# Kernel optimization log

Measured on AMD Instinct MI355X. Metric: run time of the kernel, lower is better.

The kernel has to match this reference:

```python
import jax, jax.numpy as jnp
import numpy as np

B, N, D = 16, 1024, 1152
H = 16; DH = D // H
GH = GW = 32; SY = SX = 2
WS = SY * SX                      # tokens per window
NW = (GH // SY) * (GW // SX)      # 256 windows (one dst each)
NS = NW * (WS - 1)                # 768 src tokens
NUM_PRUNE = int(N * 0.5)          # 512
NOISE_ALPHA = 0.1
SIM_BETA = 1.0


def setup_inputs() -> dict:
    key = jax.random.key(0)
    ks = jax.random.split(key, 8)
    rn = lambda k, s: jax.random.normal(k, s, jnp.float32) * 0.02
    return dict(
        x=jax.random.normal(ks[0], (B, N, D), jnp.float32),
        noise=jax.random.uniform(ks[1], (B, NW, WS), jnp.float32),
        ln1_g=jnp.ones((D,), jnp.float32), ln1_b=jnp.zeros((D,), jnp.float32),
        ln2_g=jnp.ones((D,), jnp.float32), ln2_b=jnp.zeros((D,), jnp.float32),
        w_qkv=rn(ks[2], (D, 3 * D)), b_qkv=jnp.zeros((3 * D,), jnp.float32),
        w_proj=rn(ks[3], (D, D)), b_proj=jnp.zeros((D,), jnp.float32),
        w_fc1=rn(ks[4], (D, 4 * D)), b_fc1=jnp.zeros((4 * D,), jnp.float32),
        w_fc2=rn(ks[5], (4 * D, D)), b_fc2=jnp.zeros((D,), jnp.float32),
    )


def _ln(x, g, b):
    mu = x.mean(-1, keepdims=True)
    var = ((x - mu) ** 2).mean(-1, keepdims=True)
    return (x - mu) * jax.lax.rsqrt(var + 1e-6) * g + b


def _dit_block(x, ln1_g, ln1_b, ln2_g, ln2_b, w_qkv, b_qkv, w_proj, b_proj,
               w_fc1, b_fc1, w_fc2, b_fc2):
    Bq, T, _ = x.shape
    y = _ln(x, ln1_g, ln1_b)
    q, k, v = jnp.split(y @ w_qkv + b_qkv, 3, axis=-1)
    hd = lambda t: t.reshape(Bq, T, H, DH).transpose(0, 2, 1, 3)  # [B,H,T,DH]
    q, k, v = hd(q), hd(k), hd(v)
    att = jax.nn.softmax(jnp.einsum('bhqd,bhkd->bhqk', q, k) * (1.0 / np.sqrt(DH)), axis=-1)
    o = jnp.einsum('bhqk,bhkd->bhqd', att, v).transpose(0, 2, 1, 3).reshape(Bq, T, D)
    x = x + o @ w_proj + b_proj
    y = _ln(x, ln2_g, ln2_b)
    return x + jax.nn.gelu(y @ w_fc1 + b_fc1) @ w_fc2 + b_fc2


def _sito_indices(x, noise):
    # SiTo seed (dst) selection + similarity-based prune index computation.
    xn = x / (jnp.linalg.norm(x, axis=-1, keepdims=True) + 1e-6)  # cosine feats
    grid = jnp.arange(N).reshape(GH, GW)
    win = grid.reshape(GH // SY, SY, GW // SX, SX).transpose(0, 2, 1, 3).reshape(NW, WS)
    xw = xn[:, win]                                   # [B,NW,WS,D]
    mean = xw.mean(2, keepdims=True)
    score = SIM_BETA * (xw * mean).sum(-1) + NOISE_ALPHA * noise  # [B,NW,WS]
    dst_local = jnp.argmax(score, axis=-1)            # [B,NW]
    winb = jnp.broadcast_to(win, (B, NW, WS))
    dst_idx = jnp.take_along_axis(winb, dst_local[..., None], -1)[..., 0]  # [B,NW]
    local = jnp.arange(WS)[None, None]
    keymat = jnp.where(local != dst_local[..., None], local, WS)
    src_local = jnp.sort(keymat, -1)[..., : WS - 1]   # non-dst locals, in order
    src_idx = jnp.take_along_axis(winb, src_local, -1).reshape(B, NS)
    a = jnp.take_along_axis(xn, src_idx[..., None], 1)      # [B,NS,D]
    bf = jnp.take_along_axis(xn, dst_idx[..., None], 1)     # [B,NW,D]
    sim = jnp.einsum('bsd,bnd->bsn', a, bf)                 # [B,NS,NW]
    best = jnp.argmax(sim, -1)                              # most-similar dst
    order = jnp.argsort(-jnp.max(sim, -1), axis=-1)
    pruned_pos = order[:, :NUM_PRUNE]
    kept_pos = order[:, NUM_PRUNE:]
    src_kept = jnp.take_along_axis(src_idx, kept_pos, 1)
    src_pruned = jnp.take_along_axis(src_idx, pruned_pos, 1)
    pruned_best = jnp.take_along_axis(best, pruned_pos, 1)
    return dst_idx, src_kept, src_pruned, pruned_best


def reference(x, noise, ln1_g, ln1_b, ln2_g, ln2_b, w_qkv, b_qkv, w_proj, b_proj,
              w_fc1, b_fc1, w_fc2, b_fc2):
    dst_idx, src_kept, src_pruned, pruned_best = _sito_indices(x, noise)
    keep_idx = jnp.concatenate([dst_idx, src_kept], axis=1)          # [B,Nk]
    xk = jnp.take_along_axis(x, keep_idx[..., None], 1)              # prune_fn
    out = _dit_block(xk, ln1_g, ln1_b, ln2_g, ln2_b, w_qkv, b_qkv,
                     w_proj, b_proj, w_fc1, b_fc1, w_fc2, b_fc2)

    def recover_one(o, di, sk, sp, pb):  # recover_fn: scatter + copy-from-dst
        out_dst, out_src = o[:NW], o[NW:]
        full = jnp.zeros((N, D), o.dtype)
        full = full.at[di].set(out_dst)
        full = full.at[sk].set(out_src)
        return full.at[sp].set(out_dst[pb])

    return jax.vmap(recover_one)(out, dst_idx, src_kept, src_pruned, pruned_best)
```

## Files before the change

### kernel.cpp

```cpp
#include <hip/hip_runtime.h>
#include <hip/hip_bf16.h>

namespace {

constexpr int Dd = 1152;

typedef __attribute__((ext_vector_type(8))) short bf16x8;
typedef __attribute__((ext_vector_type(4))) float f32x4;

__device__ __forceinline__ void gload_lds16(const void* g, void* l) {
  __builtin_amdgcn_global_load_lds(
      (const __attribute__((address_space(1))) void*)g,
      (__attribute__((address_space(3))) void*)l, 16, 0, 0);
}

__device__ __forceinline__ float gelu_f(float x) {
  float x3 = x * x * x;
  float z2 = 1.5957691216057308f * (x + 0.044715f * x3);
  float e = __expf(fminf(z2, 30.0f));
  return x * e / (e + 1.0f);
}

__global__ __launch_bounds__(256) void normwin_kernel(const float* __restrict__ x,
    const float* __restrict__ noise, float* __restrict__ inv,
    __hip_bfloat16* __restrict__ xnh, __hip_bfloat16* __restrict__ xnl,
    int* __restrict__ dsti, int* __restrict__ srci) {
  const int gidx = blockIdx.x;
  const int b = gidx >> 8, w = gidx & 255;
  const int wy = w >> 4, wx = w & 15;
  const int t0 = wy * 64 + wx * 2;
  const int wid = threadIdx.x >> 6, lane = threadIdx.x & 63;
  const int tok = t0 + (wid >> 1) * 32 + (wid & 1);
  const int row = (b << 10) + tok;

  const float2* xr = (const float2*)(x + (size_t)row * Dd);
  float2 v[9];
  float s = 0.f;
  #pragma unroll
  for (int e = 0; e < 9; ++e) {
    v[e] = xr[lane + 64 * e];
    s += v[e].x * v[e].x + v[e].y * v[e].y;
  }
  #pragma unroll
  for (int m = 1; m < 64; m <<= 1) s += __shfl_xor(s, m);
  float iv = 1.0f / (sqrtf(s) + 1e-6f);
  if (lane == 0) inv[row] = iv;

  __shared__ float2 xns[4][576];
  ushort2* ph = (ushort2*)(xnh + (size_t)row * Dd);
  ushort2* pl = (ushort2*)(xnl + (size_t)row * Dd);
  #pragma unroll
  for (int e = 0; e < 9; ++e) {
    float ax = v[e].x * iv, ay = v[e].y * iv;
    xns[wid][lane + 64 * e] = make_float2(ax, ay);
    __hip_bfloat16 hx = __float2bfloat16(ax), hy = __float2bfloat16(ay);
    __hip_bfloat16 lx = __float2bfloat16(ax - __bfloat162float(hx));
    __hip_bfloat16 ly = __float2bfloat16(ay - __bfloat162float(hy));
    ph[lane + 64 * e] = make_ushort2(*(ushort*)&hx, *(ushort*)&hy);
    pl[lane + 64 * e] = make_ushort2(*(ushort*)&lx, *(ushort*)&ly);
  }
  __syncthreads();

  float dot = 0.f;
  #pragma unroll
  for (int e = 0; e < 9; ++e) {
    int i = lane + 64 * e;
    float2 a0 = xns[0][i], a1 = xns[1][i], a2 = xns[2][i], a3 = xns[3][i];
    float sx = a0.x + a1.x + a2.x + a3.x;
    float sy = a0.y + a1.y + a2.y + a3.y;
    dot += (v[e].x * iv) * sx + (v[e].y * iv) * sy;
  }
  #pragma unroll
  for (int m = 1; m < 64; m <<= 1) dot += __shfl_xor(dot, m);
  __shared__ float dots[4];
  if (lane == 0) dots[wid] = dot;
  __syncthreads();
  if (threadIdx.x == 0) {
    float best = -1e30f; int bj = 0;
    #pragma unroll
    for (int j = 0; j < 4; ++j) {
      float sc = 0.25f * dots[j] + 0.1f * noise[(size_t)gidx * 4 + j];
      if (sc > best) { best = sc; bj = j; }
    }
    int tk[4] = {t0, t0 + 1, t0 + 32, t0 + 33};
    dsti[b * 256 + w] = tk[bj];
    int m = 0;
    #pragma unroll
    for (int j = 0; j < 4; ++j) if (j != bj) srci[b * 768 + w * 3 + (m++)] = tk[j];
  }
}

__global__ __launch_bounds__(256) void simgemm_kernel(
    const __hip_bfloat16* __restrict__ xnh, const __hip_bfloat16* __restrict__ xnl,
    const int* __restrict__ dsti, const int* __restrict__ srci,
    float* __restrict__ mx, int* __restrict__ best) {
  int b = blockIdx.x / 12;
  int m0 = (blockIdx.x % 12) * 64;
  __shared__ __align__(16) __hip_bfloat16 AsH[2][64 * 32];
  __shared__ __align__(16) __hip_bfloat16 AsL[2][64 * 32];
  __shared__ __align__(16) __hip_bfloat16 BsH[2][256 * 32];
  __shared__ __align__(16) __hip_bfloat16 BsL[2][256 * 32];
  const int tid = threadIdx.x, wid = tid >> 6, lane = tid & 63;
  const int g = lane >> 4, lr = lane & 15;

  const int slotRow = tid >> 2;
  const int colByte = (((tid & 3) ^ ((tid >> 3) & 3)) << 4);
  size_t aRow = (size_t)((b << 10) + srci[b * 768 + m0 + slotRow]) * Dd;
  size_t bRow[4];
  #pragma unroll
  for (int p = 0; p < 4; ++p)
    bRow[p] = (size_t)((b << 10) + dsti[b * 256 + p * 64 + slotRow]) * Dd;
  const char* xh = (const char*)xnh;
  const char* xl = (const char*)xnl;

  auto stage = [&](int buf, int k0) {
    size_t ka = (aRow + k0) * 2 + colByte;
    gload_lds16(xh + ka, (char*)AsH + buf * 4096 + wid * 1024);
    gload_lds16(xl + ka, (char*)AsL + buf * 4096 + wid * 1024);
    #pragma unroll
    for (int p = 0; p < 4; ++p) {
      size_t kb = (bRow[p] + k0) * 2 + colByte;
      gload_lds16(xh + kb, (char*)BsH + buf * 16384 + p * 4096 + wid * 1024);
      gload_lds16(xl + kb, (char*)BsL + buf * 16384 + p * 4096 + wid * 1024);
    }
  };

  f32x4 hh[16], hx[16];
  const f32x4 zf = {0.f, 0.f, 0.f, 0.f};
  #pragma unroll
  for (int nf = 0; nf < 16; ++nf) { hh[nf] = zf; hx[nf] = zf; }

  const int roff = ((g ^ ((lr >> 1) & 3)) << 3);
  stage(0, 0);
  asm volatile("s_waitcnt vmcnt(0)" ::: "memory");
  __syncthreads();
  int buf = 0;
  for (int ks = 0; ks < 36; ++ks) {
    if (ks + 1 < 36) stage(buf ^ 1, (ks + 1) * 32);
    bf16x8 ah = *(const bf16x8*)&AsH[buf][(wid * 16 + lr) * 32 + roff];
    bf16x8 al = *(const bf16x8*)&AsL[buf][(wid * 16 + lr) * 32 + roff];
    #pragma unroll
    for (int nf = 0; nf < 16; ++nf) {
      bf16x8 bh = *(const bf16x8*)&BsH[buf][(nf * 16 + lr) * 32 + roff];
      bf16x8 bl = *(const bf16x8*)&BsL[buf][(nf * 16 + lr) * 32 + roff];
      hh[nf] = __builtin_amdgcn_mfma_f32_16x16x32_bf16(ah, bh, hh[nf], 0, 0, 0);
      hx[nf] = __builtin_amdgcn_mfma_f32_16x16x32_bf16(ah, bl, hx[nf], 0, 0, 0);
      hx[nf] = __builtin_amdgcn_mfma_f32_16x16x32_bf16(al, bh, hx[nf], 0, 0, 0);
    }
    asm volatile("s_waitcnt vmcnt(0)" ::: "memory");
    __syncthreads();
    buf ^= 1;
  }

  #pragma unroll
  for (int j = 0; j < 4; ++j) {
    float bv = -1e30f; int bi = 0;
    #pragma unroll
    for (int nf = 0; nf < 16; ++nf) {
      float v = hh[nf][j] + hx[nf][j];
      if (v > bv) { bv = v; bi = nf * 16 + lr; }
    }
    #pragma unroll
    for (int m = 1; m < 16; m <<= 1) {
      float ov = __shfl_xor(bv, m);
      int oi = __shfl_xor(bi, m);
      if (ov > bv || (ov == bv && oi < bi)) { bv = ov; bi = oi; }
    }
    if (lr == 0) {
      int row = m0 + wid * 16 + g * 4 + j;
      mx[b * 768 + row] = bv;
      best[b * 768 + row] = bi;
    }
  }
}

__global__ __launch_bounds__(256) void rank_kernel(const float* __restrict__ mx,
    const int* __restrict__ best, const int* __restrict__ dsti,
    const int* __restrict__ srci, int* __restrict__ keep, int* __restrict__ srow) {
  int b = blockIdx.x;
  int tid = threadIdx.x;
  __shared__ float smx[768];
  for (int i = tid; i < 768; i += 256) smx[i] = mx[b * 768 + i];
  __syncthreads();
  if (tid < 256) {
    int t = dsti[b * 256 + tid];
    keep[b * 512 + tid] = t;
    srow[b * 1024 + t] = tid;
  }
  for (int i = tid; i < 768; i += 256) {
    float v = smx[i];
    int r = 0;
    for (int s = 0; s < 768; ++s) {
      float u = smx[s];
      r += (u > v) || (u == v && s < i);
    }
    int tok = srci[b * 768 + i];
    if (r >= 512) {
      keep[b * 512 + (r - 256)] = tok;
      srow[b * 1024 + tok] = r - 256;
    } else {
      srow[b * 1024 + tok] = best[b * 768 + i];
    }
  }
}

template<int GATHER>
__global__ __launch_bounds__(256) void ln_kernel(const float* __restrict__ xin,
    const int* __restrict__ keep, const float* __restrict__ gw,
    const float* __restrict__ bw, __hip_bfloat16* __restrict__ yout) {
  int row = blockIdx.x;
  const float* xr;
  if (GATHER) {
    int b = row >> 9, t = row & 511;
    int tok = keep[(b << 9) + t];
    xr = xin + (size_t)((b << 10) + tok) * Dd;
  } else {
    xr = xin + (size_t)row * Dd;
  }
  int tid = threadIdx.x;
  float v[5];
  float s = 0.f, s2 = 0.f;
  #pragma unroll
  for (int e = 0; e < 5; ++e) {
    int i = tid + e * 256;
    float val = (i < Dd) ? xr[i] : 0.f;
    v[e] = val; s += val; s2 += val * val;
  }
  #pragma unroll
  for (int m = 1; m < 64; m <<= 1) { s += __shfl_xor(s, m); s2 += __shfl_xor(s2, m); }
  __shared__ float ps[4], ps2[4];
  int wid = tid >> 6, lane = tid & 63;
  if (lane == 0) { ps[wid] = s; ps2[wid] = s2; }
  __syncthreads();
  s = ps[0] + ps[1] + ps[2] + ps[3];
  s2 = ps2[0] + ps2[1] + ps2[2] + ps2[3];
  constexpr float inv_d = 1.0f / Dd;
  float mu = s * inv_d;
  float var = s2 * inv_d - mu * mu;
  float rstd = rsqrtf(var + 1e-6f);
  __hip_bfloat16* yr = yout + (size_t)row * Dd;
  #pragma unroll
  for (int e = 0; e < 5; ++e) {
    int i = tid + e * 256;
    if (i < Dd) {
      yr[i] = __float2bfloat16((v[e] - mu) * rstd * gw[i] + bw[i]);
    }
  }
}

__global__ __launch_bounds__(256) void wtrans_kernel(const float* __restrict__ w,
    __hip_bfloat16* __restrict__ wT, int K, int N) {
  __shared__ float tile[32][33];
  int nt = N >> 5;
  int tk = blockIdx.x / nt, tn = blockIdx.x % nt;
  int tid = threadIdx.x;
  #pragma unroll
  for (int e = 0; e < 4; ++e) {
    int idx = tid + e * 256;
    int r = idx >> 5, c = idx & 31;
    tile[r][c] = w[(size_t)(tk * 32 + r) * N + tn * 32 + c];
  }
  __syncthreads();
  #pragma unroll
  for (int e = 0; e < 4; ++e) {
    int idx = tid + e * 256;
    int r = idx >> 5, c = idx & 31;
    wT[(size_t)(tn * 32 + r) * K + tk * 32 + c] = __float2bfloat16(tile[c][r]);
  }
}

template<int EPI>
__device__ __forceinline__ void epi_store(void* C, const float* res, int Nd,
                                          size_t row, size_t col, float v) {
  if (EPI == 0) {
    ((__hip_bfloat16*)C)[row * (size_t)Nd + col] = __float2bfloat16(v);
  } else if (EPI == 1) {
    ((float*)C)[row * (size_t)Nd + col] = v + res[row * (size_t)Nd + col];
  } else if (EPI == 2) {
    ((__hip_bfloat16*)C)[row * (size_t)Nd + col] = __float2bfloat16(gelu_f(v));
  }
}

template<int EPI>
__global__ __launch_bounds__(512, 4) void gemm128_kernel(
    const __hip_bfloat16* __restrict__ A, const __hip_bfloat16* __restrict__ BT,
    const float* __restrict__ bias, const float* __restrict__ res,
    void* __restrict__ C, int Md, int Nd, int NdPad, int Kd) {
  constexpr int BM = 128;
  __shared__ __align__(16) __hip_bfloat16 As[3][BM * 32];
  __shared__ __align__(16) __hip_bfloat16 Bs[3][256 * 32];
  const int nb = NdPad >> 8;
  const int q8 = gridDim.x >> 3;
  const int wg = (blockIdx.x & 7) * q8 + (blockIdx.x >> 3);
  const int bm = wg / nb, bnb = wg % nb;
  const int tid = threadIdx.x, wid = tid >> 6, lane = tid & 63;
  const int g = lane >> 4, lr = lane & 15;
  const int wm = wid >> 2, wn = wid & 3;
  const size_t m0 = (size_t)bm * BM, n0 = (size_t)bnb * 256;

  const int trow = tid >> 2;
  const int scol = (((tid & 3) ^ ((tid >> 3) & 3)) << 3);
  const char* Ab = (const char*)A;
  const char* Bb = (const char*)BT;

  auto stage = [&](int slot, int kt) {
    const size_t kb = ((size_t)kt << 5) + scol;
    gload_lds16(Ab + (((m0 + trow) * (size_t)Kd + kb) << 1),
                (char*)As + slot * 8192 + wid * 1024);
    gload_lds16(Bb + (((n0 + trow) * (size_t)Kd + kb) << 1),
                (char*)Bs + slot * 16384 + wid * 1024);
    gload_lds16(Bb + (((n0 + 128 + trow) * (size_t)Kd + kb) << 1),
                (char*)Bs + slot * 16384 + 8192 + wid * 1024);
  };

  f32x4 acc[4][4];
  const f32x4 zf = {0.f, 0.f, 0.f, 0.f};
  #pragma unroll
  for (int mi = 0; mi < 4; ++mi)
    #pragma unroll
    for (int ni = 0; ni < 4; ++ni) acc[mi][ni] = zf;

  const int nk = Kd >> 5;
  stage(0, 0);
  stage(1, 1);
  asm volatile("s_waitcnt vmcnt(3)" ::: "memory");
  __builtin_amdgcn_s_barrier();

  int cur = 0;
  const int roff = ((g ^ ((lr >> 1) & 3)) << 3);
  for (int kt = 0; kt < nk; ++kt) {
    const __hip_bfloat16* Ac = As[cur];
    const __hip_bfloat16* Bc = Bs[cur];
    bf16x8 af[4], bf[4];
    #pragma unroll
    for (int mi = 0; mi < 4; ++mi)
      af[mi] = *(const bf16x8*)&Ac[(wm * 64 + mi * 16 + lr) * 32 + roff];
    #pragma unroll
    for (int ni = 0; ni < 4; ++ni)
      bf[ni] = *(const bf16x8*)&Bc[(wn * 64 + ni * 16 + lr) * 32 + roff];
    if (kt + 2 < nk) stage(cur == 0 ? 2 : cur - 1, kt + 2);
    __builtin_amdgcn_s_barrier();
    __builtin_amdgcn_s_setprio(1);
    #pragma unroll
    for (int mi = 0; mi < 4; ++mi)
      #pragma unroll
      for (int ni = 0; ni < 4; ++ni)
        acc[mi][ni] = __builtin_amdgcn_mfma_f32_16x16x32_bf16(af[mi], bf[ni], acc[mi][ni], 0, 0, 0);
    __builtin_amdgcn_s_setprio(0);
    if (kt + 2 < nk)      asm volatile("s_waitcnt vmcnt(3)" ::: "memory");
    else if (kt + 1 < nk) asm volatile("s_waitcnt vmcnt(0)" ::: "memory");
    __builtin_amdgcn_s_barrier();
    cur = (cur == 2) ? 0 : cur + 1;
  }

  #pragma unroll
  for (int ni = 0; ni < 4; ++ni) {
    size_t col = n0 + wn * 64 + ni * 16 + lr;
    if (col < (size_t)Nd) {
      float bv = bias[col];
      #pragma unroll
      for (int mi = 0; mi < 4; ++mi) {
        #pragma unroll
        for (int j = 0; j < 4; ++j) {
          size_t row = m0 + wm * 64 + mi * 16 + g * 4 + j;
          float v = acc[mi][ni][j] + bv;
          epi_store<EPI>(C, res, Nd, row, col, v);
        }
      }
    }
  }
}

template<int EPI>
__global__ __launch_bounds__(256, 3) void gemm128v_kernel(
    const __hip_bfloat16* __restrict__ A, const __hip_bfloat16* __restrict__ BT,
    const float* __restrict__ bias, const float* __restrict__ res,
    const int* __restrict__ keepIdx, const float* __restrict__ xsrc,
    void* __restrict__ C, int Md, int Nd, int Kd) {
  __shared__ __align__(16) __hip_bfloat16 As[3][128 * 32];
  __shared__ __align__(16) __hip_bfloat16 Bs[3][128 * 32];
  const int nb = Nd >> 7;
  const int q8 = gridDim.x >> 3;
  const int wg = (blockIdx.x & 7) * q8 + (blockIdx.x >> 3);
  const int bm = wg / nb, bnb = wg % nb;
  const int tid = threadIdx.x, wid = tid >> 6, lane = tid & 63;
  const int g = lane >> 4, lr = lane & 15;
  const int wm = wid >> 1, wn = wid & 1;
  const size_t m0 = (size_t)bm * 128, n0 = (size_t)bnb * 128;

  const int trow = tid >> 2;
  const int scol = (((tid & 3) ^ ((tid >> 3) & 3)) << 3);
  const char* Ab = (const char*)A;
  const char* Bb = (const char*)BT;

  auto stage = [&](int slot, int kt) {
    const size_t kb = ((size_t)kt << 5) + scol;
    #pragma unroll
    for (int c = 0; c < 2; ++c)
      gload_lds16(Ab + (((m0 + c * 64 + trow) * (size_t)Kd + kb) << 1),
                  (char*)As + slot * 8192 + c * 4096 + tid * 16);
    #pragma unroll
    for (int c = 0; c < 2; ++c)
      gload_lds16(Bb + (((n0 + c * 64 + trow) * (size_t)Kd + kb) << 1),
                  (char*)Bs + slot * 8192 + c * 4096 + tid * 16);
  };

  f32x4 acc[4][4];
  const f32x4 zf = {0.f, 0.f, 0.f, 0.f};
  #pragma unroll
  for (int mi = 0; mi < 4; ++mi)
    #pragma unroll
    for (int ni = 0; ni < 4; ++ni) acc[mi][ni] = zf;

  const int roff = ((g ^ ((lr >> 1) & 3)) << 3);
  const int nk = Kd >> 5;

  bf16x8 afA[4], bfA[4], afB[4], bfB[4];

#define DSREAD(AF, BF, SLOT) { \
  const __hip_bfloat16* Ac_ = As[SLOT]; \
  const __hip_bfloat16* Bc_ = Bs[SLOT]; \
  _Pragma("unroll") for (int mi_ = 0; mi_ < 4; ++mi_) \
    AF[mi_] = *(const bf16x8*)&Ac_[(wm * 64 + mi_ * 16 + lr) * 32 + roff]; \
  _Pragma("unroll") for (int ni_ = 0; ni_ < 4; ++ni_) \
    BF[ni_] = *(const bf16x8*)&Bc_[(wn * 64 + ni_ * 16 + lr) * 32 + roff]; }

#define MFMA16(AF, BF) { \
  __builtin_amdgcn_s_setprio(1); \
  _Pragma("unroll") for (int mi_ = 0; mi_ < 4; ++mi_) \
    _Pragma("unroll") for (int ni_ = 0; ni_ < 4; ++ni_) \
      acc[mi_][ni_] = __builtin_amdgcn_mfma_f32_16x16x32_bf16(AF[mi_], BF[ni_], acc[mi_][ni_], 0, 0, 0); \
  __builtin_amdgcn_s_setprio(0); }

#define GITER(KT, S0, S1, AFC, BFC, AFN, BFN) { \
  if ((KT) <= nk - 3)      { asm volatile("s_waitcnt vmcnt(4)" ::: "memory"); } \
  else if ((KT) == nk - 2) { asm volatile("s_waitcnt vmcnt(0)" ::: "memory"); } \
  asm volatile("s_waitcnt lgkmcnt(0)" ::: "memory"); \
  __builtin_amdgcn_s_barrier(); \
  asm volatile("" ::: "memory"); \
  if ((KT) + 1 < nk) DSREAD(AFN, BFN, (S1)); \
  if ((KT) + 3 < nk) stage((S0), (KT) + 3); \
  MFMA16(AFC, BFC); }

  stage(0, 0); stage(1, 1); stage(2, 2);
  asm volatile("s_waitcnt vmcnt(8)" ::: "memory");
  __builtin_amdgcn_s_barrier();
  asm volatile("" ::: "memory");
  DSREAD(afA, bfA, 0);

  int s0 = 0, s1 = 1;
  for (int kt = 0; kt < nk; kt += 2) {
    GITER(kt, s0, s1, afA, bfA, afB, bfB);
    int s2 = (s1 == 2) ? 0 : s1 + 1;
    GITER(kt + 1, s1, s2, afB, bfB, afA, bfA);
    s0 = s2; s1 = (s2 == 2) ? 0 : s2 + 1;
  }
#undef GITER
#undef MFMA16
#undef DSREAD

  #pragma unroll
  for (int ni = 0; ni < 4; ++ni) {
    size_t col = n0 + wn * 64 + ni * 16 + lr;
    float bv = bias[col];
    #pragma unroll
    for (int mi = 0; mi < 4; ++mi) {
      #pragma unroll
      for (int j = 0; j < 4; ++j) {
        size_t row = m0 + wm * 64 + mi * 16 + g * 4 + j;
        float v = acc[mi][ni][j] + bv;
        if (EPI == 3) {
          int b = (int)(row >> 9);
          int tok = keepIdx[row];
          const float* rr = xsrc + ((size_t)(b << 10) + tok) * Dd;
          ((float*)C)[row * (size_t)Nd + col] = v + rr[col];
        } else {
          epi_store<EPI>(C, res, Nd, row, col, v);
        }
      }
    }
  }
}

__global__ __launch_bounds__(256) void vtrans_kernel(const __hip_bfloat16* __restrict__ qkv,
                                                     __hip_bfloat16* __restrict__ vT) {
  int bh = blockIdx.x;
  int b = bh >> 4, h = bh & 15;
  __shared__ __align__(16) __hip_bfloat16 Vl[256 * 72];
  int tid = threadIdx.x;
  const __hip_bfloat16 zb = __float2bfloat16(0.0f);
  for (int half = 0; half < 2; ++half) {
    __syncthreads();
    for (int idx = tid; idx < 256 * 18; idx += 256) {
      int t = idx / 18, c = idx % 18;
      *(ushort4*)&Vl[t * 72 + c * 4] =
          *(const ushort4*)&qkv[((size_t)(b * 512 + half * 256 + t)) * 3456 + 2304 + h * 72 + c * 4];
    }
    __syncthreads();
    for (int idx = tid; idx < 80 * 256; idx += 256) {
      int d = idx >> 8, t = idx & 255;
      vT[((size_t)bh * 80 + d) * 512 + half * 256 + t] = (d < 72) ? Vl[t * 72 + d] : zb;
    }
  }
}

__global__ __launch_bounds__(256) void attn_kernel(const __hip_bfloat16* __restrict__ qkv,
    const __hip_bfloat16* __restrict__ vT, __hip_bfloat16* __restrict__ o) {
  const int blk = blockIdx.x;
  const int qt = blk & 7, bh = blk >> 3;
  const int b = bh >> 4, h = bh & 15;
  __shared__ __align__(16) __hip_bfloat16 Qs[64][104];
  __shared__ __align__(16) __hip_bfloat16 Ks[64][104];
  __shared__ __align__(16) __hip_bfloat16 Vs[80][72];
  __shared__ __align__(16) __hip_bfloat16 Ps[4][16][72];
  const int tid = threadIdx.x, wid = tid >> 6, lane = tid & 63;
  const int g = lane >> 4, lr = lane & 15;
  const __hip_bfloat16 zb = __float2bfloat16(0.0f);

  for (int idx = tid; idx < 64 * 18; idx += 256) {
    int r = idx / 18, c = idx % 18;
    *(ushort4*)&Qs[r][c * 4] =
        *(const ushort4*)&qkv[((size_t)(b * 512 + qt * 64 + r)) * 3456 + h * 72 + c * 4];
  }
  for (int idx = tid; idx < 64 * 32; idx += 256) {
    int r = idx / 32, d = 72 + idx % 32;
    Qs[r][d] = zb; Ks[r][d] = zb;
  }

  f32x4 ov[5];
  const f32x4 zf = {0.f, 0.f, 0.f, 0.f};
  #pragma unroll
  for (int ni = 0; ni < 5; ++ni) ov[ni] = zf;
  float m_[4], l_[4];
  #pragma unroll
  for (int j = 0; j < 4; ++j) { m_[j] = -3.0e38f; l_[j] = 0.f; }
  const float scale = 0.11785113019775793f;

  for (int c = 0; c < 8; ++c) {
    __syncthreads();
    for (int idx = tid; idx < 64 * 18; idx += 256) {
      int r = idx / 18, cc = idx % 18;
      *(ushort4*)&Ks[r][cc * 4] =
          *(const ushort4*)&qkv[((size_t)(b * 512 + c * 64 + r)) * 3456 + 1152 + h * 72 + cc * 4];
    }
    for (int idx = tid; idx < 80 * 8; idx += 256) {
      int d = idx >> 3, t8 = idx & 7;
      *(uint4*)&Vs[d][t8 * 8] =
          *(const uint4*)&vT[((size_t)bh * 80 + d) * 512 + c * 64 + t8 * 8];
    }
    __syncthreads();

    f32x4 sf[4];
    #pragma unroll
    for (int nf = 0; nf < 4; ++nf) sf[nf] = zf;
    #pragma unroll
    for (int ks = 0; ks < 3; ++ks) {
      bf16x8 qa = *(const bf16x8*)&Qs[wid * 16 + lr][ks * 32 + g * 8];
      #pragma unroll
      for (int nf = 0; nf < 4; ++nf) {
        bf16x8 kb = *(const bf16x8*)&Ks[nf * 16 + lr][ks * 32 + g * 8];
        sf[nf] = __builtin_amdgcn_mfma_f32_16x16x32_bf16(qa, kb, sf[nf], 0, 0, 0);
      }
    }

    float cm[4];
    #pragma unroll
    for (int j = 0; j < 4; ++j)
      cm[j] = fmaxf(fmaxf(sf[0][j], sf[1][j]), fmaxf(sf[2][j], sf[3][j])) * scale;
    #pragma unroll
    for (int mm = 1; mm < 16; mm <<= 1)
      #pragma unroll
      for (int j = 0; j < 4; ++j) cm[j] = fmaxf(cm[j], __shfl_xor(cm[j], mm));
    float fac[4], rs[4];
    #pragma unroll
    for (int j = 0; j < 4; ++j) {
      float nm = fmaxf(m_[j], cm[j]);
      fac[j] = __expf(m_[j] - nm);
      m_[j] = nm;
      rs[j] = 0.f;
    }
    #pragma unroll
    for (int nf = 0; nf < 4; ++nf)
      #pragma unroll
      for (int j = 0; j < 4; ++j) {
        float pv = __expf(sf[nf][j] * scale - m_[j]);
        rs[j] += pv;
        Ps[wid][g * 4 + j][nf * 16 + lr] = __float2bfloat16(pv);
      }
    #pragma unroll
    for (int mm = 1; mm < 16; mm <<= 1)
      #pragma unroll
      for (int j = 0; j < 4; ++j) rs[j] += __shfl_xor(rs[j], mm);
    #pragma unroll
    for (int j = 0; j < 4; ++j) l_[j] = l_[j] * fac[j] + rs[j];
    #pragma unroll
    for (int ni = 0; ni < 5; ++ni)
      #pragma unroll
      for (int j = 0; j < 4; ++j) ov[ni][j] *= fac[j];

    #pragma unroll
    for (int k2 = 0; k2 < 2; ++k2) {
      bf16x8 pa = *(const bf16x8*)&Ps[wid][lr][k2 * 32 + g * 8];
      #pragma unroll
      for (int ni = 0; ni < 5; ++ni) {
        bf16x8 vb = *(const bf16x8*)&Vs[ni * 16 + lr][k2 * 32 + g * 8];
        ov[ni] = __builtin_amdgcn_mfma_f32_16x16x32_bf16(pa, vb, ov[ni], 0, 0, 0);
      }
    }
  }

  #pragma unroll
  for (int ni = 0; ni < 5; ++ni) {
    int d = ni * 16 + lr;
    if (d < 72) {
      #pragma unroll
      for (int j = 0; j < 4; ++j) {
        int t = qt * 64 + wid * 16 + g * 4 + j;
        o[((size_t)(b * 512 + t)) * 1152 + h * 72 + d] = __float2bfloat16(ov[ni][j] / l_[j]);
      }
    }
  }
}

__global__ __launch_bounds__(256) void recover_kernel(const float* __restrict__ yout,
    const int* __restrict__ srow, float* __restrict__ out) {
  int idx = blockIdx.x * 256 + threadIdx.x;
  int q = idx % 288;
  int bnv = idx / 288;
  int r = srow[bnv];
  int b = bnv >> 10;
  const float4* src = (const float4*)yout + ((size_t)((b << 9) + r)) * 288 + q;
  ((float4*)out)[idx] = *src;
}

}

extern "C" void kernel_launch(void* const* d_in, const int* in_sizes, int n_in,
                              void* d_out, int out_size, void* d_ws, size_t ws_size,
                              hipStream_t stream) {
  (void)in_sizes; (void)n_in; (void)out_size; (void)ws_size;
  const float* x      = (const float*)d_in[0];
  const float* noise  = (const float*)d_in[1];
  const float* ln1_g  = (const float*)d_in[2];
  const float* ln1_b  = (const float*)d_in[3];
  const float* ln2_g  = (const float*)d_in[4];
  const float* ln2_b  = (const float*)d_in[5];
  const float* w_qkv  = (const float*)d_in[6];
  const float* b_qkv  = (const float*)d_in[7];
  const float* w_proj = (const float*)d_in[8];
  const float* b_proj = (const float*)d_in[9];
  const float* w_fc1  = (const float*)d_in[10];
  const float* b_fc1  = (const float*)d_in[11];
  const float* w_fc2  = (const float*)d_in[12];
  const float* b_fc2  = (const float*)d_in[13];
  float* out = (float*)d_out;

  char* p = (char*)d_ws;
  auto alloc = [&](size_t bytes) {
    char* r = p;
    p += (bytes + 255) & ~(size_t)255;
    return r;
  };
  __hip_bfloat16* wqkvT  = (__hip_bfloat16*)alloc((size_t)3584 * 1152 * 2);
  __hip_bfloat16* wprojT = (__hip_bfloat16*)alloc((size_t)1280 * 1152 * 2);
  __hip_bfloat16* wfc1T  = (__hip_bfloat16*)alloc((size_t)4608 * 1152 * 2);
  __hip_bfloat16* wfc2T  = (__hip_bfloat16*)alloc((size_t)1280 * 4608 * 2);
  float* inv = (float*)alloc(16384 * 4);
  int* dsti  = (int*)alloc(4096 * 4);
  int* srci  = (int*)alloc(12288 * 4);
  float* mx  = (float*)alloc(12288 * 4);
  int* best  = (int*)alloc(12288 * 4);
  int* keep  = (int*)alloc(8192 * 4);
  int* srow  = (int*)alloc(16384 * 4);
  float* yout = (float*)alloc((size_t)8192 * 1152 * 4);
  __hip_bfloat16* y1   = (__hip_bfloat16*)alloc((size_t)8192 * 1152 * 2);
  __hip_bfloat16* qkvb = (__hip_bfloat16*)alloc((size_t)8192 * 4608 * 2);
  __hip_bfloat16* vT   = (__hip_bfloat16*)alloc((size_t)256 * 80 * 512 * 2);
  __hip_bfloat16* ob   = (__hip_bfloat16*)alloc((size_t)8192 * 1152 * 2);
  float* x2 = (float*)alloc((size_t)8192 * 1152 * 4);

  __hip_bfloat16* xnh = qkvb;
  __hip_bfloat16* xnl = qkvb + (size_t)16 * 1024 * 1152;

  wtrans_kernel<<<36 * 108, 256, 0, stream>>>(w_qkv, wqkvT, 1152, 3456);
  wtrans_kernel<<<36 * 36, 256, 0, stream>>>(w_proj, wprojT, 1152, 1152);
  wtrans_kernel<<<36 * 144, 256, 0, stream>>>(w_fc1, wfc1T, 1152, 4608);
  wtrans_kernel<<<144 * 36, 256, 0, stream>>>(w_fc2, wfc2T, 4608, 1152);

  normwin_kernel<<<4096, 256, 0, stream>>>(x, noise, inv, xnh, xnl, dsti, srci);
  simgemm_kernel<<<16 * 12, 256, 0, stream>>>(xnh, xnl, dsti, srci, mx, best);
  rank_kernel<<<16, 256, 0, stream>>>(mx, best, dsti, srci, keep, srow);

  ln_kernel<1><<<8192, 256, 0, stream>>>(x, keep, ln1_g, ln1_b, y1);
  gemm128_kernel<0><<<64 * 14, 512, 0, stream>>>(y1, wqkvT, b_qkv, nullptr,
                                                 qkvb, 8192, 3456, 3584, 1152);
  vtrans_kernel<<<256, 256, 0, stream>>>(qkvb, vT);
  attn_kernel<<<2048, 256, 0, stream>>>(qkvb, vT, ob);
  gemm128v_kernel<3><<<64 * 9, 256, 0, stream>>>(ob, wprojT, b_proj, nullptr, keep, x,
                                                 x2, 8192, 1152, 1152);
  ln_kernel<0><<<8192, 256, 0, stream>>>(x2, nullptr, ln2_g, ln2_b, y1);
  gemm128v_kernel<2><<<64 * 36, 256, 0, stream>>>(y1, wfc1T, b_fc1, nullptr, nullptr, nullptr,
                                                  qkvb, 8192, 4608, 1152);
  gemm128v_kernel<1><<<64 * 9, 256, 0, stream>>>(qkvb, wfc2T, b_fc2, x2, nullptr, nullptr,
                                                 yout, 8192, 1152, 4608);

  recover_kernel<<<18432, 256, 0, stream>>>(yout, srow, out);
}
```

Before: 734.2 us.

## Fuse V transpose into QKV GEMM epilogue and merge weight-transpose launches

The QKV GEMM epilogue now writes the V columns directly into the transposed per-head vT layout, so the separate vtrans kernel is removed. The attention kernel zero-fills the padded V rows in shared memory and loads only the 72 real rows. The four weight-transpose launches are merged into one launch that dispatches on block index. This saves a full read and write of V plus some launch overhead. The cost is scattered, strided stores of V in the GEMM epilogue, which may coalesce poorly.

```diff
diff --git a/kernel.cpp b/kernel.cpp
--- a/kernel.cpp
+++ b/kernel.cpp
@@ -248,11 +248,20 @@
   }
 }
 
-__global__ __launch_bounds__(256) void wtrans_kernel(const float* __restrict__ w,
-    __hip_bfloat16* __restrict__ wT, int K, int N) {
+__global__ __launch_bounds__(256) void wtrans_all_kernel(
+    const float* __restrict__ w0, __hip_bfloat16* __restrict__ o0,
+    const float* __restrict__ w1, __hip_bfloat16* __restrict__ o1,
+    const float* __restrict__ w2, __hip_bfloat16* __restrict__ o2,
+    const float* __restrict__ w3, __hip_bfloat16* __restrict__ o3) {
   __shared__ float tile[32][33];
+  int bid = blockIdx.x;
+  const float* w; __hip_bfloat16* wT; int K, N, local;
+  if (bid < 3888)       { w = w0; wT = o0; K = 1152; N = 3456; local = bid; }
+  else if (bid < 5184)  { w = w1; wT = o1; K = 1152; N = 1152; local = bid - 3888; }
+  else if (bid < 10368) { w = w2; wT = o2; K = 1152; N = 4608; local = bid - 5184; }
+  else                  { w = w3; wT = o3; K = 4608; N = 1152; local = bid - 10368; }
   int nt = N >> 5;
-  int tk = blockIdx.x / nt, tn = blockIdx.x % nt;
+  int tk = local / nt, tn = local % nt;
   int tid = threadIdx.x;
   #pragma unroll
   for (int e = 0; e < 4; ++e) {
@@ -285,6 +294,7 @@
 __global__ __launch_bounds__(512, 4) void gemm128_kernel(
     const __hip_bfloat16* __restrict__ A, const __hip_bfloat16* __restrict__ BT,
     const float* __restrict__ bias, const float* __restrict__ res,
+    __hip_bfloat16* __restrict__ vTout,
     void* __restrict__ C, int Md, int Nd, int NdPad, int Kd) {
   constexpr int BM = 128;
   __shared__ __align__(16) __hip_bfloat16 As[3][BM * 32];
@@ -358,13 +368,32 @@
     size_t col = n0 + wn * 64 + ni * 16 + lr;
     if (col < (size_t)Nd) {
       float bv = bias[col];
-      #pragma unroll
-      for (int mi = 0; mi < 4; ++mi) {
+      if (EPI == 4 && col >= 2304) {
+        int vc = (int)col - 2304;
+        int h = vc / 72, d = vc % 72;
         #pragma unroll
-        for (int j = 0; j < 4; ++j) {
-          size_t row = m0 + wm * 64 + mi * 16 + g * 4 + j;
-          float v = acc[mi][ni][j] + bv;
-          epi_store<EPI>(C, res, Nd, row, col, v);
+        for (int mi = 0; mi < 4; ++mi) {
+          #pragma unroll
+          for (int j = 0; j < 4; ++j) {
+            size_t row = m0 + wm * 64 + mi * 16 + g * 4 + j;
+            int bb = (int)(row >> 9), t = (int)(row & 511);
+            vTout[(((size_t)(bb * 16 + h)) * 80 + d) * 512 + t] =
+                __float2bfloat16(acc[mi][ni][j] + bv);
+          }
+        }
+      } else {
+        #pragma unroll
+        for (int mi = 0; mi < 4; ++mi) {
+          #pragma unroll
+          for (int j = 0; j < 4; ++j) {
+            size_t row = m0 + wm * 64 + mi * 16 + g * 4 + j;
+            float v = acc[mi][ni][j] + bv;
+            if (EPI == 4) {
+              ((__hip_bfloat16*)C)[row * (size_t)Nd + col] = __float2bfloat16(v);
+            } else {
+              epi_store<EPI>(C, res, Nd, row, col, v);
+            }
+          }
         }
       }
     }
@@ -482,28 +511,6 @@
   }
 }
 
-__global__ __launch_bounds__(256) void vtrans_kernel(const __hip_bfloat16* __restrict__ qkv,
-                                                     __hip_bfloat16* __restrict__ vT) {
-  int bh = blockIdx.x;
-  int b = bh >> 4, h = bh & 15;
-  __shared__ __align__(16) __hip_bfloat16 Vl[256 * 72];
-  int tid = threadIdx.x;
-  const __hip_bfloat16 zb = __float2bfloat16(0.0f);
-  for (int half = 0; half < 2; ++half) {
-    __syncthreads();
-    for (int idx = tid; idx < 256 * 18; idx += 256) {
-      int t = idx / 18, c = idx % 18;
-      *(ushort4*)&Vl[t * 72 + c * 4] =
-          *(const ushort4*)&qkv[((size_t)(b * 512 + half * 256 + t)) * 3456 + 2304 + h * 72 + c * 4];
-    }
-    __syncthreads();
-    for (int idx = tid; idx < 80 * 256; idx += 256) {
-      int d = idx >> 8, t = idx & 255;
-      vT[((size_t)bh * 80 + d) * 512 + half * 256 + t] = (d < 72) ? Vl[t * 72 + d] : zb;
-    }
-  }
-}
-
 __global__ __launch_bounds__(256) void attn_kernel(const __hip_bfloat16* __restrict__ qkv,
     const __hip_bfloat16* __restrict__ vT, __hip_bfloat16* __restrict__ o) {
   const int blk = blockIdx.x;
@@ -526,6 +533,9 @@
     int r = idx / 32, d = 72 + idx % 32;
     Qs[r][d] = zb; Ks[r][d] = zb;
   }
+  for (int idx = tid; idx < 8 * 72; idx += 256) {
+    Vs[72 + idx / 72][idx % 72] = zb;
+  }
 
   f32x4 ov[5];
   const f32x4 zf = {0.f, 0.f, 0.f, 0.f};
@@ -543,7 +553,7 @@
       *(ushort4*)&Ks[r][cc * 4] =
           *(const ushort4*)&qkv[((size_t)(b * 512 + c * 64 + r)) * 3456 + 1152 + h * 72 + cc * 4];
     }
-    for (int idx = tid; idx < 80 * 8; idx += 256) {
+    for (int idx = tid; idx < 72 * 8; idx += 256) {
       int d = idx >> 3, t8 = idx & 7;
       *(uint4*)&Vs[d][t8 * 8] =
           *(const uint4*)&vT[((size_t)bh * 80 + d) * 512 + c * 64 + t8 * 8];
@@ -682,19 +692,16 @@
   __hip_bfloat16* xnh = qkvb;
   __hip_bfloat16* xnl = qkvb + (size_t)16 * 1024 * 1152;
 
-  wtrans_kernel<<<36 * 108, 256, 0, stream>>>(w_qkv, wqkvT, 1152, 3456);
-  wtrans_kernel<<<36 * 36, 256, 0, stream>>>(w_proj, wprojT, 1152, 1152);
-  wtrans_kernel<<<36 * 144, 256, 0, stream>>>(w_fc1, wfc1T, 1152, 4608);
-  wtrans_kernel<<<144 * 36, 256, 0, stream>>>(w_fc2, wfc2T, 4608, 1152);
+  wtrans_all_kernel<<<15552, 256, 0, stream>>>(w_qkv, wqkvT, w_proj, wprojT,
+                                               w_fc1, wfc1T, w_fc2, wfc2T);
 
   normwin_kernel<<<4096, 256, 0, stream>>>(x, noise, inv, xnh, xnl, dsti, srci);
   simgemm_kernel<<<16 * 12, 256, 0, stream>>>(xnh, xnl, dsti, srci, mx, best);
   rank_kernel<<<16, 256, 0, stream>>>(mx, best, dsti, srci, keep, srow);
 
   ln_kernel<1><<<8192, 256, 0, stream>>>(x, keep, ln1_g, ln1_b, y1);
-  gemm128_kernel<0><<<64 * 14, 512, 0, stream>>>(y1, wqkvT, b_qkv, nullptr,
+  gemm128_kernel<4><<<64 * 14, 512, 0, stream>>>(y1, wqkvT, b_qkv, nullptr, vT,
                                                  qkvb, 8192, 3456, 3584, 1152);
-  vtrans_kernel<<<256, 256, 0, stream>>>(qkvb, vT);
   attn_kernel<<<2048, 256, 0, stream>>>(qkvb, vT, ob);
   gemm128v_kernel<3><<<64 * 9, 256, 0, stream>>>(ob, wprojT, b_proj, nullptr, keep, x,
                                                  x2, 8192, 1152, 1152);
```

Result: faster. 700.6 us (-4.6%).
